# Performance work log

Measured on AMD Instinct MI355X. Metric: run time of the kernel, lower is better.

## Reference

```python
import jax, jax.numpy as jnp
import numpy as np

N, C, H, W = 128, 3, 256, 256
MAXNORM = 5.371920351148152
MAX_SQ = 16  # static bound for data-dependent squaring loop
PADE_B = [6.476475253248e+16, 3.238237626624e+16, 7771770303897600.0,
          1187353796428800.0, 129060195264000.0, 10559470521600.0,
          670442572800.0, 33522128640.0, 1323241920.0, 40840800.0,
          960960.0, 16380.0, 182.0, 1.0]


def pade13(A):
    b = PADE_B
    I = jnp.eye(A.shape[-1], dtype=A.dtype)
    A2 = A @ A
    A4 = A2 @ A2
    A6 = A4 @ A2
    U = A @ (A6 @ (b[13] * A6 + b[11] * A4 + b[9] * A2)
             + b[7] * A6 + b[5] * A4 + b[3] * A2 + b[1] * I)
    V = (A6 @ (b[12] * A6 + b[10] * A4 + b[8] * A2)
         + b[6] * A6 + b[4] * A4 + b[2] * A2 + b[0] * I)
    return U, V


def expm_affine(theta):  # theta: [N,2,3] -> exp of padded 3x3, top 2 rows
    n = theta.shape[0]
    A = jnp.concatenate([theta, jnp.zeros((n, 1, 3), theta.dtype)], axis=1)
    fro = jnp.sqrt(jnp.sum(A * A, axis=(1, 2), keepdims=True))
    n_sq = jnp.maximum(0.0, jnp.ceil(jnp.log2(fro / MAXNORM)))
    Asc = A / (2.0 ** n_sq)
    U, V = pade13(Asc)
    R = jnp.linalg.solve(U + V, -U + V)
    k = n_sq.reshape(n).astype(jnp.int32)
    def body(i, Rc):
        return jnp.where((i < k)[:, None, None], jnp.matmul(Rc, Rc), Rc)
    R = jax.lax.fori_loop(0, MAX_SQ, body, R)
    return R[:, :2, :]


def affine_grid(theta, Ho, Wo):  # align_corners=True
    xs = jnp.linspace(-1.0, 1.0, Wo, dtype=theta.dtype)
    ys = jnp.linspace(-1.0, 1.0, Ho, dtype=theta.dtype)
    gy, gx = jnp.meshgrid(ys, xs, indexing='ij')          # [Ho,Wo]
    base = jnp.stack([gx, gy, jnp.ones_like(gx)], axis=-1)  # [Ho,Wo,3]
    return jnp.einsum('hwk,nck->nhwc', base, theta)        # [N,Ho,Wo,2]


def grid_sample(x, grid):  # bilinear, zeros padding, align_corners=True
    _, _, Hi, Wi = x.shape
    ix = (grid[..., 0] + 1.0) * 0.5 * (Wi - 1)
    iy = (grid[..., 1] + 1.0) * 0.5 * (Hi - 1)
    ix0 = jnp.floor(ix)
    iy0 = jnp.floor(iy)
    ix1 = ix0 + 1.0
    iy1 = iy0 + 1.0
    wx1 = ix - ix0; wx0 = 1.0 - wx1
    wy1 = iy - iy0; wy0 = 1.0 - wy1

    def gather(yy, xx):
        valid = ((yy >= 0) & (yy < Hi) & (xx >= 0) & (xx < Wi))
        yc = jnp.clip(yy, 0, Hi - 1).astype(jnp.int32)
        xc = jnp.clip(xx, 0, Wi - 1).astype(jnp.int32)
        vals = jax.vmap(lambda img, y, xi: img[:, y, xi])(x, yc, xc)  # [N,C,Ho,Wo]
        return vals * valid[:, None].astype(x.dtype)

    return (gather(iy0, ix0) * (wy0 * wx0)[:, None]
            + gather(iy0, ix1) * (wy0 * wx1)[:, None]
            + gather(iy1, ix0) * (wy1 * wx0)[:, None]
            + gather(iy1, ix1) * (wy1 * wx1)[:, None])


def setup_inputs() -> dict:
    key = jax.random.key(0)
    k1, k2 = jax.random.split(key)
    x = jax.random.normal(k1, (N, C, H, W), dtype=jnp.float32)
    theta = 0.1 * jax.random.normal(k2, (N, 6), dtype=jnp.float32)
    return {"x": x, "theta": theta}


def reference(x, theta):
    th = expm_affine(theta.reshape(-1, 2, 3))  # [N,2,3]
    grid = affine_grid(th, H, W)               # [N,H,W,2]
    return grid_sample(x, grid)                # [N,C,H,W]
```

## Files before the change

### kernel.cpp

```cpp
#include <hip/hip_runtime.h>

#define Ndim 128
#define Cdim 3
#define Hdim 256
#define Wdim 256
#define HW (Hdim * Wdim)
#define MAXNORM_F 5.371920351148152f

typedef float vf2 __attribute__((ext_vector_type(2)));
typedef unsigned int uint32;

__device__ __forceinline__ void mm3f(const float a[3][3], const float b[3][3], float c[3][3]) {
    #pragma unroll
    for (int i = 0; i < 3; ++i)
        #pragma unroll
        for (int j = 0; j < 3; ++j) {
            float s = 0.0f;
            #pragma unroll
            for (int k = 0; k < 3; ++k) s = fmaf(a[i][k], b[k][j], s);
            c[i][j] = s;
        }
}

__global__ void expm_kernel(const float* __restrict__ theta, float* __restrict__ thOut) {
    int n = blockIdx.x * blockDim.x + threadIdx.x;
    if (n >= Ndim) return;

    const float b[14] = {6.476475253248e+16f, 3.238237626624e+16f, 7771770303897600.0f,
                         1187353796428800.0f, 129060195264000.0f, 10559470521600.0f,
                         670442572800.0f, 33522128640.0f, 1323241920.0f, 40840800.0f,
                         960960.0f, 16380.0f, 182.0f, 1.0f};

    float A[3][3];
    #pragma unroll
    for (int j = 0; j < 3; ++j) {
        A[0][j] = theta[n * 6 + j];
        A[1][j] = theta[n * 6 + 3 + j];
        A[2][j] = 0.0f;
    }

    float fro2 = 0.0f;
    #pragma unroll
    for (int i = 0; i < 3; ++i)
        #pragma unroll
        for (int j = 0; j < 3; ++j) fro2 = fmaf(A[i][j], A[i][j], fro2);
    float fro = sqrtf(fro2);

    float nsq = fmaxf(0.0f, ceilf(log2f(fro / MAXNORM_F)));
    int k = (int)nsq;
    float sc = exp2f(-nsq);
    #pragma unroll
    for (int i = 0; i < 3; ++i)
        #pragma unroll
        for (int j = 0; j < 3; ++j) A[i][j] *= sc;

    float A2[3][3], A4[3][3], A6[3][3], P[3][3], Wm[3][3], T[3][3], U[3][3], V[3][3];
    mm3f(A, A, A2);
    mm3f(A2, A2, A4);
    mm3f(A4, A2, A6);

    #pragma unroll
    for (int i = 0; i < 3; ++i)
        #pragma unroll
        for (int j = 0; j < 3; ++j)
            P[i][j] = b[13] * A6[i][j] + b[11] * A4[i][j] + b[9] * A2[i][j];
    mm3f(A6, P, T);
    #pragma unroll
    for (int i = 0; i < 3; ++i)
        #pragma unroll
        for (int j = 0; j < 3; ++j)
            Wm[i][j] = T[i][j] + b[7] * A6[i][j] + b[5] * A4[i][j] + b[3] * A2[i][j]
                       + (i == j ? b[1] : 0.0f);
    mm3f(A, Wm, U);

    #pragma unroll
    for (int i = 0; i < 3; ++i)
        #pragma unroll
        for (int j = 0; j < 3; ++j)
            P[i][j] = b[12] * A6[i][j] + b[10] * A4[i][j] + b[8] * A2[i][j];
    mm3f(A6, P, T);
    #pragma unroll
    for (int i = 0; i < 3; ++i)
        #pragma unroll
        for (int j = 0; j < 3; ++j)
            V[i][j] = T[i][j] + b[6] * A6[i][j] + b[4] * A4[i][j] + b[2] * A2[i][j]
                      + (i == j ? b[0] : 0.0f);

    float M[3][6];
    #pragma unroll
    for (int i = 0; i < 3; ++i)
        #pragma unroll
        for (int j = 0; j < 3; ++j) {
            M[i][j]     = U[i][j] + V[i][j];
            M[i][j + 3] = V[i][j] - U[i][j];
        }
    #pragma unroll
    for (int col = 0; col < 3; ++col) {
        int piv = col;
        float best = fabsf(M[col][col]);
        for (int r = col + 1; r < 3; ++r) {
            float v = fabsf(M[r][col]);
            if (v > best) { best = v; piv = r; }
        }
        if (piv != col) {
            #pragma unroll
            for (int j = 0; j < 6; ++j) {
                float t = M[col][j]; M[col][j] = M[piv][j]; M[piv][j] = t;
            }
        }
        float inv = 1.0f / M[col][col];
        #pragma unroll
        for (int j = 0; j < 6; ++j) M[col][j] *= inv;
        #pragma unroll
        for (int r = 0; r < 3; ++r) {
            if (r == col) continue;
            float f = M[r][col];
            #pragma unroll
            for (int j = 0; j < 6; ++j) M[r][j] -= f * M[col][j];
        }
    }
    float R[3][3];
    #pragma unroll
    for (int i = 0; i < 3; ++i)
        #pragma unroll
        for (int j = 0; j < 3; ++j) R[i][j] = M[i][j + 3];

    for (int i = 0; i < 16; ++i) {
        if (i < k) {
            float Rn[3][3];
            mm3f(R, R, Rn);
            #pragma unroll
            for (int a = 0; a < 3; ++a)
                #pragma unroll
                for (int c = 0; c < 3; ++c) R[a][c] = Rn[a][c];
        }
    }

    #pragma unroll
    for (int j = 0; j < 3; ++j) {
        thOut[n * 6 + j]     = (float)R[0][j];
        thOut[n * 6 + 3 + j] = (float)R[1][j];
    }
}

__global__ __launch_bounds__(256) void sample_kernel(const float* __restrict__ x,
                                                     const float* __restrict__ th,
                                                     float* __restrict__ out) {
    __shared__ float lds[10240];

    const int nwg_per_xcd = 8192 / 8;
    int bid = blockIdx.x;
    int wgid = (bid & 7) * nwg_per_xcd + (bid >> 3);

    int tw  = wgid & 7;
    int thp = (wgid >> 3) & 7;
    int n   = wgid >> 6;

    int tid = threadIdx.x;
    int w  = (tw << 5) + (tid & 31);
    int h0 = (thp << 5) + ((tid >> 5) << 2);

    const float* t = th + n * 6;
    float t0 = t[0], t1 = t[1], t2 = t[2], t3 = t[3], t4 = t[4], t5 = t[5];

    float Cx = 127.5f * (t2 - t0 - t1 + 1.0f);
    float Cy = 127.5f * (t5 - t3 - t4 + 1.0f);

    float fwA = (float)(tw << 5),  fwB = fwA + 31.0f;
    float fhA = (float)(thp << 5), fhB = fhA + 31.0f;
    float xlo = fminf(fwA * t0, fwB * t0) + fminf(fhA * t1, fhB * t1) + Cx;
    float xhi = fmaxf(fwA * t0, fwB * t0) + fmaxf(fhA * t1, fhB * t1) + Cx;
    float ylo = fminf(fwA * t3, fwB * t3) + fminf(fhA * t4, fhB * t4) + Cy;
    float yhi = fmaxf(fwA * t3, fwB * t3) + fmaxf(fhA * t4, fhB * t4) + Cy;
    int Xlo = (int)floorf(xlo) - 1, Xhi = (int)floorf(xhi) + 2;
    int Ylo = (int)floorf(ylo) - 1, Yhi = (int)floorf(yhi) + 2;
    int cn = Xhi - Xlo + 1;
    int rn = Yhi - Ylo + 1;

    size_t nbase = (size_t)n * Cdim * HW;

    float ixs[4], iys[4];
    float ixb = fmaf((float)w, t0, fmaf((float)h0, t1, Cx));
    float iyb = fmaf((float)w, t3, fmaf((float)h0, t4, Cy));
    #pragma unroll
    for (int p = 0; p < 4; ++p) {
        ixs[p] = fmaf((float)p, t1, ixb);
        iys[p] = fmaf((float)p, t4, iyb);
    }

    bool fast = (cn <= 52) && (rn <= 55) && (rn >= 1) && (cn >= 1);

    if (fast) {
        int bxw = (min(max(Xlo, 0), Wdim - 56)) & ~3;
        int byw = min(max(Ylo, 0), Hdim - rn);

        int totc  = 42 * (rn + 1);
        int iters = (totc + 255) >> 8;
        const float* gbase = x + nbase;
        for (int it = 0; it < iters; ++it) {
            int c = (it << 8) + tid;
            int row = c / 42;
            int rem = c - row * 42;
            row = min(row, rn);
            int ch   = rem / 14;
            int colc = rem - ch * 14;
            int srow = min(byw + row, Hdim - 1);
            const float* gp = gbase + (size_t)ch * HW + (srow << 8) + bxw + (colc << 2);
            __builtin_amdgcn_global_load_lds(
                (const __attribute__((address_space(1))) uint32*)gp,
                (__attribute__((address_space(3))) uint32*)((uint32*)lds + ((size_t)c << 2)),
                16, 0, 0);
        }
        __syncthreads();

        bool interior = (Xlo >= 0) && (Xhi <= Wdim - 1) && (Ylo >= 0) && (Yhi <= Hdim - 1);

        float res[4][3];
        if (interior) {
            #pragma unroll
            for (int p = 0; p < 4; ++p) {
                float ix = ixs[p], iy = iys[p];
                float fx = floorf(ix), fy = floorf(iy);
                int x0i = (int)fx, y0i = (int)fy;
                float wx1 = ix - fx, wx0 = 1.0f - wx1;
                float wy1 = iy - fy, wy0 = 1.0f - wy1;

                int lx = x0i - bxw;
                int ly = y0i - byw;
                int base = ly * 168 + lx;
                #pragma unroll
                for (int c = 0; c < Cdim; ++c) {
                    const float* bp = lds + base + c * 56;
                    float v00 = bp[0],   v01 = bp[1];
                    float v10 = bp[168], v11 = bp[169];
                    float top = fmaf(v01, wx1, v00 * wx0);
                    float bot = fmaf(v11, wx1, v10 * wx0);
                    res[p][c] = fmaf(wy1, bot, wy0 * top);
                }
            }
        } else {
            #pragma unroll
            for (int p = 0; p < 4; ++p) {
                float ix = ixs[p], iy = iys[p];
                float fx = floorf(ix), fy = floorf(iy);
                int x0i = (int)fx, y0i = (int)fy;
                float wx1 = ix - fx, wx0 = 1.0f - wx1;
                float wy1 = iy - fy, wy0 = 1.0f - wy1;
                float mx0 = ((unsigned)x0i       < (unsigned)Wdim) ? 1.0f : 0.0f;
                float mx1 = ((unsigned)(x0i + 1) < (unsigned)Wdim) ? 1.0f : 0.0f;
                float my0 = ((unsigned)y0i       < (unsigned)Hdim) ? 1.0f : 0.0f;
                float my1 = ((unsigned)(y0i + 1) < (unsigned)Hdim) ? 1.0f : 0.0f;
                float wxm0 = wx0 * mx0, wxm1 = wx1 * mx1;
                float wym0 = wy0 * my0, wym1 = wy1 * my1;

                int lx0 = min(max(x0i - bxw, 0), 55);
                int lx1 = min(max(x0i + 1 - bxw, 0), 55);
                int ly0 = min(max(y0i - byw, 0), rn);
                int ly1 = min(max(y0i + 1 - byw, 0), rn);
                int r0 = ly0 * 168, r1 = ly1 * 168;
                #pragma unroll
                for (int c = 0; c < Cdim; ++c) {
                    int b0 = r0 + c * 56;
                    int b1 = r1 + c * 56;
                    float v00 = lds[b0 + lx0], v01 = lds[b0 + lx1];
                    float v10 = lds[b1 + lx0], v11 = lds[b1 + lx1];
                    float top = fmaf(v01, wxm1, v00 * wxm0);
                    float bot = fmaf(v11, wxm1, v10 * wxm0);
                    res[p][c] = fmaf(wym1, bot, wym0 * top);
                }
            }
        }

        size_t p0 = (size_t)h0 * Wdim + w;
        #pragma unroll
        for (int c = 0; c < Cdim; ++c)
            #pragma unroll
            for (int p = 0; p < 4; ++p)
                __builtin_nontemporal_store(res[p][c],
                    out + nbase + (size_t)c * HW + p0 + (size_t)p * Wdim);
    } else {
        const float* img0 = x + nbase;
        #pragma unroll
        for (int p = 0; p < 4; ++p) {
            float ix = ixs[p], iy = iys[p];
            float fx = floorf(ix), fy = floorf(iy);
            int ix0 = (int)fx, iy0 = (int)fy;
            float wx1 = ix - fx, wx0 = 1.0f - wx1;
            float wy1 = iy - fy, wy0 = 1.0f - wy1;
            float mx0 = ((unsigned)ix0       < (unsigned)Wdim) ? 1.0f : 0.0f;
            float mx1 = ((unsigned)(ix0 + 1) < (unsigned)Wdim) ? 1.0f : 0.0f;
            float my0 = ((unsigned)iy0       < (unsigned)Hdim) ? 1.0f : 0.0f;
            float my1 = ((unsigned)(iy0 + 1) < (unsigned)Hdim) ? 1.0f : 0.0f;
            int xc0 = min(max(ix0, 0), Wdim - 1);
            int xc1 = min(max(ix0 + 1, 0), Wdim - 1);
            int yc0 = min(max(iy0, 0), Hdim - 1);
            int yc1 = min(max(iy0 + 1, 0), Hdim - 1);
            float w00 = wy0 * wx0 * my0 * mx0;
            float w01 = wy0 * wx1 * my0 * mx1;
            float w10 = wy1 * wx0 * my1 * mx0;
            float w11 = wy1 * wx1 * my1 * mx1;
            int o00 = yc0 * Wdim + xc0, o01 = yc0 * Wdim + xc1;
            int o10 = yc1 * Wdim + xc0, o11 = yc1 * Wdim + xc1;
            #pragma unroll
            for (int c = 0; c < Cdim; ++c) {
                const float* img = img0 + (size_t)c * HW;
                float r = fmaf(img[o00], w00, fmaf(img[o01], w01,
                          fmaf(img[o10], w10, img[o11] * w11)));
                out[nbase + (size_t)c * HW + (size_t)(h0 + p) * Wdim + w] = r;
            }
        }
    }
}

extern "C" void kernel_launch(void* const* d_in, const int* in_sizes, int n_in,
                              void* d_out, int out_size, void* d_ws, size_t ws_size,
                              hipStream_t stream) {
    const float* x     = (const float*)d_in[0];
    const float* theta = (const float*)d_in[1];
    float* out = (float*)d_out;
    float* th  = (float*)d_ws;

    expm_kernel<<<1, 128, 0, stream>>>(theta, th);

    int nblocks = 8192;
    sample_kernel<<<nblocks, 256, 0, stream>>>(x, th, out);
}
```

Before: 40.87 us.

## Double-buffer per-channel LDS staging to overlap loads with sampling

Instead of staging all three channels of the input patch into shared memory at once, the sample kernel now stages one channel at a time into two alternating LDS buffers. The load for the next channel is issued before sampling the current one, and results are stored per channel. The goal is to hide global-to-LDS latency behind interpolation work and to shrink the LDS footprint, which allows more resident workgroups. The cost is extra barriers, and the fast-path row limit tightens to 48, which could send more tiles to the slower direct-gather path.

```diff
diff --git a/kernel.cpp b/kernel.cpp
--- a/kernel.cpp
+++ b/kernel.cpp
@@ -7,6 +7,10 @@
 #define HW (Hdim * Wdim)
 #define MAXNORM_F 5.371920351148152f
 
+#define LCOLS 56
+#define LROWS 48
+#define LBUF  (LCOLS * LROWS)
+
 typedef float vf2 __attribute__((ext_vector_type(2)));
 typedef unsigned int uint32;
 
@@ -146,7 +150,7 @@
 __global__ __launch_bounds__(256) void sample_kernel(const float* __restrict__ x,
                                                      const float* __restrict__ th,
                                                      float* __restrict__ out) {
-    __shared__ float lds[10240];
+    __shared__ float lds[2][LBUF];
 
     const int nwg_per_xcd = 8192 / 8;
     int bid = blockIdx.x;
@@ -188,57 +192,68 @@
         iys[p] = fmaf((float)p, t4, iyb);
     }
 
-    bool fast = (cn <= 52) && (rn <= 55) && (rn >= 1) && (cn >= 1);
+    bool fast = (cn <= 52) && (rn <= LROWS) && (rn >= 1) && (cn >= 1);
 
     if (fast) {
-        int bxw = (min(max(Xlo, 0), Wdim - 56)) & ~3;
+        int bxw = (min(max(Xlo, 0), Wdim - LCOLS)) & ~3;
         int byw = min(max(Ylo, 0), Hdim - rn);
-
-        int totc  = 42 * (rn + 1);
-        int iters = (totc + 255) >> 8;
+        int totc = 14 * rn;
         const float* gbase = x + nbase;
-        for (int it = 0; it < iters; ++it) {
-            int c = (it << 8) + tid;
-            int row = c / 42;
-            int rem = c - row * 42;
-            row = min(row, rn);
-            int ch   = rem / 14;
-            int colc = rem - ch * 14;
-            int srow = min(byw + row, Hdim - 1);
-            const float* gp = gbase + (size_t)ch * HW + (srow << 8) + bxw + (colc << 2);
-            __builtin_amdgcn_global_load_lds(
-                (const __attribute__((address_space(1))) uint32*)gp,
-                (__attribute__((address_space(3))) uint32*)((uint32*)lds + ((size_t)c << 2)),
-                16, 0, 0);
-        }
-        __syncthreads();
+
+        auto stage = [&](int ch, int buf) {
+            #pragma unroll
+            for (int it = 0; it < 3; ++it) {
+                int k = (it << 8) + tid;
+                if (k < totc) {
+                    int row = k / 14;
+                    int col = k - row * 14;
+                    const float* gp = gbase + (size_t)ch * HW
+                                    + ((byw + row) << 8) + bxw + (col << 2);
+                    __builtin_amdgcn_global_load_lds(
+                        (const __attribute__((address_space(1))) uint32*)gp,
+                        (__attribute__((address_space(3))) uint32*)
+                            ((uint32*)&lds[buf][0] + ((size_t)k << 2)),
+                        16, 0, 0);
+                }
+            }
+        };
 
         bool interior = (Xlo >= 0) && (Xhi <= Wdim - 1) && (Ylo >= 0) && (Yhi <= Hdim - 1);
 
-        float res[4][3];
+        stage(0, 0);
+
+        int   basev[4];
+        float wx1v[4], wy1v[4];
         if (interior) {
             #pragma unroll
             for (int p = 0; p < 4; ++p) {
                 float ix = ixs[p], iy = iys[p];
                 float fx = floorf(ix), fy = floorf(iy);
-                int x0i = (int)fx, y0i = (int)fy;
-                float wx1 = ix - fx, wx0 = 1.0f - wx1;
-                float wy1 = iy - fy, wy0 = 1.0f - wy1;
-
-                int lx = x0i - bxw;
-                int ly = y0i - byw;
-                int base = ly * 168 + lx;
-                #pragma unroll
-                for (int c = 0; c < Cdim; ++c) {
-                    const float* bp = lds + base + c * 56;
-                    float v00 = bp[0],   v01 = bp[1];
-                    float v10 = bp[168], v11 = bp[169];
-                    float top = fmaf(v01, wx1, v00 * wx0);
-                    float bot = fmaf(v11, wx1, v10 * wx0);
-                    res[p][c] = fmaf(wy1, bot, wy0 * top);
-                }
-            }
-        } else {
+                wx1v[p] = ix - fx;
+                wy1v[p] = iy - fy;
+                basev[p] = ((int)fy - byw) * LCOLS + ((int)fx - bxw);
+            }
+        }
+        size_t p0 = (size_t)h0 * Wdim + w;
+
+        auto sample_interior = [&](int buf, int c) {
+            float* o = out + nbase + (size_t)c * HW + p0;
+            #pragma unroll
+            for (int p = 0; p < 4; ++p) {
+                const float* bp = &lds[buf][basev[p]];
+                float v00 = bp[0],     v01 = bp[1];
+                float v10 = bp[LCOLS], v11 = bp[LCOLS + 1];
+                float wx1 = wx1v[p], wx0 = 1.0f - wx1;
+                float wy1 = wy1v[p], wy0 = 1.0f - wy1;
+                float top = fmaf(v01, wx1, v00 * wx0);
+                float bot = fmaf(v11, wx1, v10 * wx0);
+                __builtin_nontemporal_store(fmaf(wy1, bot, wy0 * top),
+                                            o + (size_t)p * Wdim);
+            }
+        };
+
+        auto sample_edge = [&](int buf, int c) {
+            float* o = out + nbase + (size_t)c * HW + p0;
             #pragma unroll
             for (int p = 0; p < 4; ++p) {
                 float ix = ixs[p], iy = iys[p];
@@ -253,31 +268,28 @@
                 float wxm0 = wx0 * mx0, wxm1 = wx1 * mx1;
                 float wym0 = wy0 * my0, wym1 = wy1 * my1;
 
-                int lx0 = min(max(x0i - bxw, 0), 55);
-                int lx1 = min(max(x0i + 1 - bxw, 0), 55);
-                int ly0 = min(max(y0i - byw, 0), rn);
-                int ly1 = min(max(y0i + 1 - byw, 0), rn);
-                int r0 = ly0 * 168, r1 = ly1 * 168;
-                #pragma unroll
-                for (int c = 0; c < Cdim; ++c) {
-                    int b0 = r0 + c * 56;
-                    int b1 = r1 + c * 56;
-                    float v00 = lds[b0 + lx0], v01 = lds[b0 + lx1];
-                    float v10 = lds[b1 + lx0], v11 = lds[b1 + lx1];
-                    float top = fmaf(v01, wxm1, v00 * wxm0);
-                    float bot = fmaf(v11, wxm1, v10 * wxm0);
-                    res[p][c] = fmaf(wym1, bot, wym0 * top);
-                }
-            }
-        }
-
-        size_t p0 = (size_t)h0 * Wdim + w;
-        #pragma unroll
-        for (int c = 0; c < Cdim; ++c)
-            #pragma unroll
-            for (int p = 0; p < 4; ++p)
-                __builtin_nontemporal_store(res[p][c],
-                    out + nbase + (size_t)c * HW + p0 + (size_t)p * Wdim);
+                int lx0 = min(max(x0i - bxw, 0), LCOLS - 1);
+                int lx1 = min(max(x0i + 1 - bxw, 0), LCOLS - 1);
+                int ly0 = min(max(y0i - byw, 0), rn - 1);
+                int ly1 = min(max(y0i + 1 - byw, 0), rn - 1);
+                const float* B = &lds[buf][0];
+                float v00 = B[ly0 * LCOLS + lx0], v01 = B[ly0 * LCOLS + lx1];
+                float v10 = B[ly1 * LCOLS + lx0], v11 = B[ly1 * LCOLS + lx1];
+                float top = fmaf(v01, wxm1, v00 * wxm0);
+                float bot = fmaf(v11, wxm1, v10 * wxm0);
+                __builtin_nontemporal_store(fmaf(wym1, bot, wym0 * top),
+                                            o + (size_t)p * Wdim);
+            }
+        };
+
+        __syncthreads();
+        stage(1, 1);
+        if (interior) sample_interior(0, 0); else sample_edge(0, 0);
+        __syncthreads();
+        stage(2, 0);
+        if (interior) sample_interior(1, 1); else sample_edge(1, 1);
+        __syncthreads();
+        if (interior) sample_interior(0, 2); else sample_edge(0, 2);
     } else {
         const float* img0 = x + nbase;
         #pragma unroll
```

Measured after the change: 41.30 us. About the same (+1.1%).
